# Kernel tuning notes

Measured on AMD Instinct MI355X. Metric: run time of the kernel, lower is better.

The kernel has to match this reference:

```python
import jax, jax.numpy as jnp
import numpy as np
from jax import lax

T, N, E = 12, 10000, 160000
C_IN, C_H, C_OUT = 32, 64, 32
EPS = 1e-5


def _glorot(key, shape):
    fan_in, fan_out = shape[-2] if len(shape) > 1 else shape[0], shape[-1]
    s = (6.0 / (fan_in + fan_out)) ** 0.5
    return jax.random.uniform(key, shape, jnp.float32, -s, s)


def setup_inputs() -> dict:
    key = jax.random.key(0)
    ks = jax.random.split(key, 16)
    inp = {
        "x": jax.random.normal(ks[0], (T, N, C_IN), jnp.float32),
        "edge_index": jax.random.randint(ks[1], (2, E), 0, N, jnp.int32),
        "edge_weight": jax.random.uniform(ks[2], (E,), jnp.float32),
        # layer 1 (input layer): in=C_IN -> C_H
        "conv_w1": _glorot(ks[3], (C_H, C_IN, 3)) * 0.1,
        "conv_b1": jnp.zeros((C_H,), jnp.float32),
        "gamma1": jnp.ones((C_H,), jnp.float32),
        "beta1": jnp.zeros((C_H,), jnp.float32),
        "gcn_w1": _glorot(ks[4], (C_H, C_H)),
        "gcn_b1": jnp.zeros((C_H,), jnp.float32),
        # layer 2 (hidden layer): C_H -> C_H
        "conv_w2": _glorot(ks[5], (C_H, C_H, 3)) * 0.1,
        "conv_b2": jnp.zeros((C_H,), jnp.float32),
        "gamma2": jnp.ones((C_H,), jnp.float32),
        "beta2": jnp.zeros((C_H,), jnp.float32),
        "gcn_w2": _glorot(ks[6], (C_H, C_H)),
        "gcn_b2": jnp.zeros((C_H,), jnp.float32),
        # output linear: C_H -> C_OUT
        "out_w": _glorot(ks[7], (C_H, C_OUT)),
        "out_b": jnp.zeros((C_OUT,), jnp.float32),
    }
    return inp


def _stgcn_layer(x, edge_index, edge_weight, cw, cb, gamma, beta, gw, gb):
    # x: [T, N, C_in]  ->  torch.stack(x).permute(1,2,0) = [N, C_in, T]
    xs = jnp.transpose(x, (1, 2, 0))
    h = lax.conv_general_dilated(xs, cw, (1,), [(1, 1)],
                                 dimension_numbers=("NCH", "OIH", "NCH"))
    h = h + cb[None, :, None]
    # InstanceNorm1d(affine) over the temporal dim
    mu = h.mean(-1, keepdims=True)
    var = ((h - mu) ** 2).mean(-1, keepdims=True)
    h = (h - mu) * lax.rsqrt(var + EPS) * gamma[None, :, None] + beta[None, :, None]
    h = jax.nn.relu(h)
    h = jnp.transpose(h, (2, 0, 1))  # [T, N, C_out]
    # GCNConv per timestep (vectorized over T)
    src, dst = edge_index[0], edge_index[1]
    n = h.shape[1]
    deg = jnp.zeros((n,), h.dtype).at[dst].add(edge_weight) + 1.0  # self-loop weight 1
    dis = lax.rsqrt(deg)
    norm = dis[src] * edge_weight * dis[dst]  # [E]
    xw = jnp.einsum("tnc,cd->tnd", h, gw)  # [T, N, C_out]
    msg = xw[:, src, :] * norm[None, :, None]  # [T, E, C_out]
    agg = jax.vmap(lambda m: jax.ops.segment_sum(m, dst, num_segments=n))(msg)
    agg = agg + (dis * dis)[None, :, None] * xw + gb  # self loop + bias
    return agg


def reference(x, edge_index, edge_weight,
              conv_w1, conv_b1, gamma1, beta1, gcn_w1, gcn_b1,
              conv_w2, conv_b2, gamma2, beta2, gcn_w2, gcn_b2,
              out_w, out_b):
    h = _stgcn_layer(x, edge_index, edge_weight,
                     conv_w1, conv_b1, gamma1, beta1, gcn_w1, gcn_b1)
    h = _stgcn_layer(h, edge_index, edge_weight,
                     conv_w2, conv_b2, gamma2, beta2, gcn_w2, gcn_b2)
    out = jnp.einsum("tnc,co->tno", h, out_w) + out_b  # per-t linear
    return out.mean(axis=0)  # [N, C_OUT]
```

## Files before the change

kernel.cpp:

```cpp
#include <hip/hip_runtime.h>
#include <hip/hip_bf16.h>
#include <stdint.h>

#define MAXDEG 64

typedef short s16x8 __attribute__((ext_vector_type(8)));
typedef short s16x4 __attribute__((ext_vector_type(4)));
typedef float f32x4 __attribute__((ext_vector_type(4)));

static __device__ __forceinline__ float us2f(unsigned short u) {
    union { float f; unsigned int i; } cv; cv.i = ((unsigned int)u) << 16; return cv.f;
}
static __device__ __forceinline__ unsigned short f2us(float f) {
    __hip_bfloat16 h = __float2bfloat16(f);
    return *(unsigned short*)&h;
}

__global__ void k_build_ell(const int* __restrict__ ei, const float* __restrict__ ew,
                            float* __restrict__ deg, unsigned* __restrict__ cnt,
                            int2* __restrict__ ell, int E)
{
    int e = blockIdx.x * 256 + threadIdx.x;
    if (e >= E) return;
    int s = ei[e], d = ei[E + e];
    float w = ew[e];
    atomicAdd(&deg[d], w);
    unsigned slot = atomicAdd(&cnt[d], 1u);
    if (slot < MAXDEG) ell[(size_t)d * MAXDEG + slot] = make_int2(s, __float_as_int(w));
}

__global__ void k_norm(int2* __restrict__ ell, const unsigned* __restrict__ cnt,
                       const float* __restrict__ deg, int N)
{
    int idx = blockIdx.x * 256 + threadIdx.x;
    if (idx >= N * MAXDEG) return;
    int n = idx >> 6;
    int s = idx & (MAXDEG - 1);
    unsigned dg = cnt[n]; if (dg > MAXDEG) dg = MAXDEG;
    int sxo = 0; float nrm = 0.f;
    if ((unsigned)s < dg) {
        int2 p = ell[idx];
        unsigned sx = (unsigned)p.x;
        if (sx < (unsigned)N) {
            nrm = rsqrtf(deg[sx] + 1.0f) * __int_as_float(p.y) * rsqrtf(deg[n] + 1.0f);
            sxo = p.x;
        }
    }
    ell[idx] = make_int2(sxo, __float_as_int(nrm));
}

static __device__ __forceinline__ void edge_acc(float* __restrict__ a, float nrm,
                                                const unsigned short* __restrict__ qp)
{
    ushort4 w0 = *(const ushort4*)qp;
    ushort4 w1 = *(const ushort4*)(qp + 256);
    ushort4 w2 = *(const ushort4*)(qp + 512);
    a[0] = fmaf(nrm, us2f(w0.x), a[0]);  a[1] = fmaf(nrm, us2f(w0.y), a[1]);
    a[2] = fmaf(nrm, us2f(w0.z), a[2]);  a[3] = fmaf(nrm, us2f(w0.w), a[3]);
    a[4] = fmaf(nrm, us2f(w1.x), a[4]);  a[5] = fmaf(nrm, us2f(w1.y), a[5]);
    a[6] = fmaf(nrm, us2f(w1.z), a[6]);  a[7] = fmaf(nrm, us2f(w1.w), a[7]);
    a[8] = fmaf(nrm, us2f(w2.x), a[8]);  a[9] = fmaf(nrm, us2f(w2.y), a[9]);
    a[10] = fmaf(nrm, us2f(w2.z), a[10]); a[11] = fmaf(nrm, us2f(w2.w), a[11]);
}

template<int CIN>
__global__ __launch_bounds__(512, 4) void k_layer_a(
    const float* __restrict__ x_in,
    const float* __restrict__ cw,
    const float* __restrict__ gm, const float* __restrict__ bt,
    const float* __restrict__ gw,
    unsigned short* __restrict__ xw_out, int N)
{
    constexpr int KT   = CIN / 32;
    constexpr int WSTR = (CIN == 64) ? 72 : 40;
    __shared__ __align__(16) short WT[3 * 64 * WSTR];
    __shared__ __align__(16) short gwT[64 * 72];
    __shared__ __align__(16) short xh[8][14 * 72];

    const int tid = threadIdx.x;
    const int nn = tid >> 6;
    const int c = tid & 63;
    const int m = c & 15;
    const int q = c >> 4;
    const int mrow = (m < 12) ? m : 11;
    int n = blockIdx.x * 8 + nn;
    if (n >= N) n = N - 1;

    for (int g = tid; g < 3 * 64 * CIN; g += 512) {
        int kk = g / (64 * CIN);
        int r = g - kk * 64 * CIN;
        int cc = r / CIN, ci = r - cc * CIN;
        WT[kk * (64 * WSTR) + cc * WSTR + ci] = (short)f2us(cw[(cc * CIN + ci) * 3 + kk]);
    }
    for (int g = tid; g < 4096; g += 512) {
        int cc = g >> 6, d = g & 63;
        gwT[d * 72 + cc] = (short)f2us(gw[g]);
    }
    #pragma unroll
    for (int it = 0; it < (12 * CIN) / 64; ++it) {
        int i = it * 64 + c;
        int t = i / CIN, ci = i - t * CIN;
        xh[nn][(t + 1) * 72 + ci] = (short)f2us(x_in[((size_t)t * N + n) * CIN + ci]);
    }
    if (c < CIN) { xh[nn][c] = 0; xh[nn][13 * 72 + c] = 0; }
    __syncthreads();

    f32x4 acc[4];
    #pragma unroll
    for (int nt = 0; nt < 4; ++nt) acc[nt] = (f32x4){0.f, 0.f, 0.f, 0.f};
    #pragma unroll
    for (int kk = 0; kk < 3; ++kk) {
        #pragma unroll
        for (int kt = 0; kt < KT; ++kt) {
            s16x8 aA = *(const s16x8*)&xh[nn][(mrow + kk) * 72 + kt * 32 + q * 8];
            #pragma unroll
            for (int nt = 0; nt < 4; ++nt) {
                s16x8 bB = *(const s16x8*)&WT[kk * (64 * WSTR) + (nt * 16 + m) * WSTR + kt * 32 + q * 8];
                acc[nt] = __builtin_amdgcn_mfma_f32_16x16x32_bf16(aA, bB, acc[nt], 0, 0, 0);
            }
        }
    }

    #pragma unroll
    for (int nt = 0; nt < 4; ++nt) {
        float s  = acc[nt][0] + acc[nt][1] + acc[nt][2] + acc[nt][3];
        float s2 = acc[nt][0] * acc[nt][0] + acc[nt][1] * acc[nt][1]
                 + acc[nt][2] * acc[nt][2] + acc[nt][3] * acc[nt][3];
        if (q == 3) { s = 0.f; s2 = 0.f; }
        s  += __shfl_xor(s, 16);  s  += __shfl_xor(s, 32);
        s2 += __shfl_xor(s2, 16); s2 += __shfl_xor(s2, 32);
        const float mu  = s * (1.f / 12.f);
        const float var = s2 * (1.f / 12.f) - mu * mu;
        const float scn = rsqrtf(var + 1e-5f) * gm[nt * 16 + m];
        const float sbn = bt[nt * 16 + m];
        if (q < 3) {
            #pragma unroll
            for (int reg = 0; reg < 4; ++reg) {
                float h = fmaf(acc[nt][reg] - mu, scn, sbn);
                h = h > 0.f ? h : 0.f;
                xh[nn][(q * 4 + reg) * 72 + nt * 16 + m] = (short)f2us(h);
            }
        }
    }

    s16x8 a2[2];
    #pragma unroll
    for (int kt2 = 0; kt2 < 2; ++kt2)
        a2[kt2] = *(const s16x8*)&xh[nn][mrow * 72 + kt2 * 32 + q * 8];
    f32x4 acc2[4];
    #pragma unroll
    for (int nt = 0; nt < 4; ++nt) acc2[nt] = (f32x4){0.f, 0.f, 0.f, 0.f};
    #pragma unroll
    for (int nt = 0; nt < 4; ++nt) {
        #pragma unroll
        for (int kt2 = 0; kt2 < 2; ++kt2) {
            s16x8 b2 = *(const s16x8*)&gwT[(nt * 16 + m) * 72 + kt2 * 32 + q * 8];
            acc2[nt] = __builtin_amdgcn_mfma_f32_16x16x32_bf16(a2[kt2], b2, acc2[nt], 0, 0, 0);
        }
    }

    unsigned short* dst = xw_out + (size_t)n * 768;
    if (q < 3) {
        #pragma unroll
        for (int nt = 0; nt < 4; ++nt)
            #pragma unroll
            for (int reg = 0; reg < 4; ++reg)
                dst[(q * 4 + reg) * 64 + nt * 16 + m] = f2us(acc2[nt][reg]);
    }
}

__global__ __launch_bounds__(512, 4) void k_gather_a(
    const unsigned short* __restrict__ xw_in,
    const int2* __restrict__ ell, const unsigned* __restrict__ cnt,
    const float* __restrict__ deg, const float* __restrict__ gb,
    const float* __restrict__ cw,
    const float* __restrict__ gm, const float* __restrict__ bt,
    const float* __restrict__ gw,
    unsigned short* __restrict__ rowmean, int N)
{
    constexpr int WSTR = 72;
    __shared__ __align__(16) short WT[3 * 64 * WSTR];
    __shared__ __align__(16) short gwT[64 * 72];
    __shared__ __align__(16) short xh[8][14 * 72];

    const int tid = threadIdx.x;
    const int nn = tid >> 6;
    const int L = tid & 63;
    const int m = L & 15;
    const int q = L >> 4;
    const int mrow = (m < 12) ? m : 11;

    for (int g = tid; g < 3 * 64 * 64; g += 512) {
        int kk = g >> 12;
        int r = g & 4095;
        int cc = r >> 6, ci = r & 63;
        WT[kk * (64 * WSTR) + cc * WSTR + ci] = (short)f2us(cw[(cc * 64 + ci) * 3 + kk]);
    }
    for (int g = tid; g < 4096; g += 512) {
        int cc = g >> 6, d = g & 63;
        gwT[d * 72 + cc] = (short)f2us(gw[g]);
    }
    xh[nn][13 * 72 + L] = 0;
    __syncthreads();

    int base = blockIdx.x * 16 + nn * 2;
    unsigned nP[2];
    nP[0] = (unsigned)((base     < N) ? base     : N - 1);
    nP[1] = (unsigned)((base + 1 < N) ? base + 1 : N - 1);

    float aP[2][12];
    #pragma unroll
    for (int j = 0; j < 2; ++j) {
        const unsigned n = nP[j];
        const float dn = rsqrtf(deg[n] + 1.0f);
        const float d2 = dn * dn;
        const unsigned short* self = xw_in + (size_t)n * 768 + L * 4;
        ushort4 v0 = *(const ushort4*)self;
        ushort4 v1 = *(const ushort4*)(self + 256);
        ushort4 v2 = *(const ushort4*)(self + 512);
        const int c0 = (L * 4) & 63;
        const float g0 = gb[c0], g1 = gb[c0 + 1], g2 = gb[c0 + 2], g3 = gb[c0 + 3];
        float* a = aP[j];
        a[0] = fmaf(d2, us2f(v0.x), g0); a[1] = fmaf(d2, us2f(v0.y), g1);
        a[2] = fmaf(d2, us2f(v0.z), g2); a[3] = fmaf(d2, us2f(v0.w), g3);
        a[4] = fmaf(d2, us2f(v1.x), g0); a[5] = fmaf(d2, us2f(v1.y), g1);
        a[6] = fmaf(d2, us2f(v1.z), g2); a[7] = fmaf(d2, us2f(v1.w), g3);
        a[8] = fmaf(d2, us2f(v2.x), g0); a[9] = fmaf(d2, us2f(v2.y), g1);
        a[10] = fmaf(d2, us2f(v2.z), g2); a[11] = fmaf(d2, us2f(v2.w), g3);
    }
    {
        unsigned dg0 = cnt[nP[0]]; if (dg0 > MAXDEG) dg0 = MAXDEG;
        unsigned dg1 = cnt[nP[1]]; if (dg1 > MAXDEG) dg1 = MAXDEG;
        unsigned dgm = dg0 > dg1 ? dg0 : dg1;
        const int2* r0 = ell + (size_t)nP[0] * MAXDEG;
        const int2* r1 = ell + (size_t)nP[1] * MAXDEG;
        unsigned e = 0;
        for (; e + 2 <= dgm; e += 2) {
            int2 p00 = r0[e], p01 = r0[e + 1], p10 = r1[e], p11 = r1[e + 1];
            edge_acc(aP[0], __int_as_float(p00.y), xw_in + (size_t)(unsigned)p00.x * 768 + L * 4);
            edge_acc(aP[1], __int_as_float(p10.y), xw_in + (size_t)(unsigned)p10.x * 768 + L * 4);
            edge_acc(aP[0], __int_as_float(p01.y), xw_in + (size_t)(unsigned)p01.x * 768 + L * 4);
            edge_acc(aP[1], __int_as_float(p11.y), xw_in + (size_t)(unsigned)p11.x * 768 + L * 4);
        }
        if (e < dgm) {
            int2 p00 = r0[e], p10 = r1[e];
            edge_acc(aP[0], __int_as_float(p00.y), xw_in + (size_t)(unsigned)p00.x * 768 + L * 4);
            edge_acc(aP[1], __int_as_float(p10.y), xw_in + (size_t)(unsigned)p10.x * 768 + L * 4);
        }
    }

    #pragma unroll
    for (int j = 0; j < 2; ++j) {
        const unsigned n = nP[j];
        const float* a = aP[j];

        xh[nn][L] = 0;
        #pragma unroll
        for (int j3 = 0; j3 < 3; ++j3) {
            s16x4 s4 = { (short)f2us(a[j3 * 4 + 0]), (short)f2us(a[j3 * 4 + 1]),
                         (short)f2us(a[j3 * 4 + 2]), (short)f2us(a[j3 * 4 + 3]) };
            *(s16x4*)&xh[nn][(j3 * 4 + q + 1) * 72 + ((L * 4) & 63)] = s4;
        }

        f32x4 acc[4];
        #pragma unroll
        for (int nt = 0; nt < 4; ++nt) acc[nt] = (f32x4){0.f, 0.f, 0.f, 0.f};
        #pragma unroll
        for (int kk = 0; kk < 3; ++kk) {
            #pragma unroll
            for (int kt = 0; kt < 2; ++kt) {
                s16x8 aA = *(const s16x8*)&xh[nn][(mrow + kk) * 72 + kt * 32 + q * 8];
                #pragma unroll
                for (int nt = 0; nt < 4; ++nt) {
                    s16x8 bB = *(const s16x8*)&WT[kk * (64 * WSTR) + (nt * 16 + m) * WSTR + kt * 32 + q * 8];
                    acc[nt] = __builtin_amdgcn_mfma_f32_16x16x32_bf16(aA, bB, acc[nt], 0, 0, 0);
                }
            }
        }

        #pragma unroll
        for (int nt = 0; nt < 4; ++nt) {
            float s  = acc[nt][0] + acc[nt][1] + acc[nt][2] + acc[nt][3];
            float s2 = acc[nt][0] * acc[nt][0] + acc[nt][1] * acc[nt][1]
                     + acc[nt][2] * acc[nt][2] + acc[nt][3] * acc[nt][3];
            if (q == 3) { s = 0.f; s2 = 0.f; }
            s  += __shfl_xor(s, 16);  s  += __shfl_xor(s, 32);
            s2 += __shfl_xor(s2, 16); s2 += __shfl_xor(s2, 32);
            const float mu  = s * (1.f / 12.f);
            const float var = s2 * (1.f / 12.f) - mu * mu;
            const float scn = rsqrtf(var + 1e-5f) * gm[nt * 16 + m];
            const float sbn = bt[nt * 16 + m];
            if (q < 3) {
                #pragma unroll
                for (int reg = 0; reg < 4; ++reg) {
                    float h = fmaf(acc[nt][reg] - mu, scn, sbn);
                    h = h > 0.f ? h : 0.f;
                    xh[nn][(q * 4 + reg) * 72 + nt * 16 + m] = (short)f2us(h);
                }
            }
        }

        s16x8 a2[2];
        #pragma unroll
        for (int kt2 = 0; kt2 < 2; ++kt2)
            a2[kt2] = *(const s16x8*)&xh[nn][mrow * 72 + kt2 * 32 + q * 8];
        f32x4 acc2[4];
        #pragma unroll
        for (int nt = 0; nt < 4; ++nt) acc2[nt] = (f32x4){0.f, 0.f, 0.f, 0.f};
        #pragma unroll
        for (int nt = 0; nt < 4; ++nt) {
            #pragma unroll
            for (int kt2 = 0; kt2 < 2; ++kt2) {
                s16x8 b2 = *(const s16x8*)&gwT[(nt * 16 + m) * 72 + kt2 * 32 + q * 8];
                acc2[nt] = __builtin_amdgcn_mfma_f32_16x16x32_bf16(a2[kt2], b2, acc2[nt], 0, 0, 0);
            }
        }

        #pragma unroll
        for (int nt = 0; nt < 4; ++nt) {
            float pm = (q < 3) ? (acc2[nt][0] + acc2[nt][1] + acc2[nt][2] + acc2[nt][3]) : 0.f;
            pm += __shfl_xor(pm, 16); pm += __shfl_xor(pm, 32);
            if (q == 0)
                rowmean[(size_t)n * 64 + nt * 16 + m] = f2us(pm * (1.f / 12.f));
        }
    }
}

__global__ __launch_bounds__(256) void k_final(
    const unsigned short* __restrict__ rowmean, const int2* __restrict__ ell,
    const unsigned* __restrict__ cnt, const float* __restrict__ deg,
    const float* __restrict__ gb,
    const float* __restrict__ ow, const float* __restrict__ ob,
    float* __restrict__ dout, int N)
{
    __shared__ __align__(16) float hbuf[4][64];
    const int tid = threadIdx.x;
    const int nn = tid >> 6, L = tid & 63;
    int n = blockIdx.x * 4 + nn;
    if (n >= N) n = N - 1;
    const float dn = rsqrtf(deg[n] + 1.0f);
    const float d2 = dn * dn;

    float a = fmaf(d2, us2f(rowmean[(size_t)n * 64 + L]), gb[L]);

    unsigned dg = cnt[n]; if (dg > MAXDEG) dg = MAXDEG;
    const int2* row = ell + (size_t)n * MAXDEG;
    unsigned e = 0;
    for (; e + 8 <= dg; e += 8) {
        #pragma unroll
        for (int i = 0; i < 8; ++i) {
            int2 p = row[e + i];
            a = fmaf(__int_as_float(p.y), us2f(rowmean[(size_t)(unsigned)p.x * 64 + L]), a);
        }
    }
    for (; e < dg; ++e) {
        int2 p = row[e];
        a = fmaf(__int_as_float(p.y), us2f(rowmean[(size_t)(unsigned)p.x * 64 + L]), a);
    }

    hbuf[nn][L] = a;
    __syncthreads();
    if (L < 32) {
        float oa = ob[L];
        #pragma unroll
        for (int cc = 0; cc < 64; ++cc)
            oa = fmaf(hbuf[nn][cc], ow[cc * 32 + L], oa);
        dout[(size_t)n * 32 + L] = oa;
    }
}

extern "C" void kernel_launch(void* const* d_in, const int* in_sizes, int n_in,
                              void* d_out, int out_size, void* d_ws, size_t ws_size,
                              hipStream_t stream)
{
    const float* x   = (const float*)d_in[0];
    const int*   ei  = (const int*)d_in[1];
    const float* ew  = (const float*)d_in[2];
    const float* cw1 = (const float*)d_in[3];
    const float* gm1 = (const float*)d_in[5];
    const float* bt1 = (const float*)d_in[6];
    const float* gw1 = (const float*)d_in[7];
    const float* gb1 = (const float*)d_in[8];
    const float* cw2 = (const float*)d_in[9];
    const float* gm2 = (const float*)d_in[11];
    const float* bt2 = (const float*)d_in[12];
    const float* gw2 = (const float*)d_in[13];
    const float* gb2 = (const float*)d_in[14];
    const float* ow  = (const float*)d_in[15];
    const float* ob  = (const float*)d_in[16];

    const int N = in_sizes[0] / (12 * 32);
    const int E = in_sizes[2];

    char* p0 = (char*)d_ws;
    char* p = p0;
    float* deg = (float*)p;          p += (size_t)N * 4;
    unsigned* cnt = (unsigned*)p;    p += (size_t)N * 4;
    p = (char*)(((uintptr_t)p + 255) & ~(uintptr_t)255);
    int2* ell = (int2*)p;            p += (size_t)N * MAXDEG * 8;
    p = (char*)(((uintptr_t)p + 255) & ~(uintptr_t)255);
    unsigned short* bufXW1 = (unsigned short*)p; p += (size_t)N * 768 * 2;
    unsigned short* rowmean = (unsigned short*)p; p += (size_t)N * 64 * 2;

    const size_t need = (size_t)(p - p0);
    if (ws_size < need) {
        hipMemsetAsync(d_out, 0, (size_t)out_size * 4, stream);
        return;
    }

    hipMemsetAsync(deg, 0, (size_t)N * 8, stream);

    const int eb   = (E + 255) / 256;
    const int nb8  = (N + 7) / 8;
    const int nb16 = (N + 15) / 16;
    const int nb4  = (N + 3) / 4;
    k_build_ell<<<eb, 256, 0, stream>>>(ei, ew, deg, cnt, ell, E);
    k_norm<<<(N * MAXDEG + 255) / 256, 256, 0, stream>>>(ell, cnt, deg, N);

    k_layer_a<32><<<nb8, 512, 0, stream>>>(x, cw1, gm1, bt1, gw1, bufXW1, N);
    k_gather_a<<<nb16, 512, 0, stream>>>(bufXW1, ell, cnt, deg, gb1,
                                         cw2, gm2, bt2, gw2, rowmean, N);
    k_final<<<nb4, 256, 0, stream>>>(rowmean, ell, cnt, deg, gb2, ow, ob, (float*)d_out, N);
}
```

Measured before the change: 196.7 us.

## Use persistent grid-stride blocks and batched 8-edge gather in layer kernels

Both MFMA layer kernels now launch a fixed grid (1024 and 768 blocks) and loop over node groups grid-stride, so the per-block staging of conv and GCN weights into LDS is paid once per block, not once per small node group. The gather kernel now assigns one node per wavefront instead of two, and walks the padded ELL row in chunks of 8 edges with all loads issued before the FMAs, to raise memory-level parallelism. Padding to a multiple of 8 relies on the zeroed padding entries in the ELL table, which adds some wasted loads of row 0. The fixed grid sizes may leave the GPU underfilled or unevenly loaded.

```diff
diff --git a/kernel.cpp b/kernel.cpp
--- a/kernel.cpp
+++ b/kernel.cpp
@@ -49,20 +49,6 @@
     ell[idx] = make_int2(sxo, __float_as_int(nrm));
 }
 
-static __device__ __forceinline__ void edge_acc(float* __restrict__ a, float nrm,
-                                                const unsigned short* __restrict__ qp)
-{
-    ushort4 w0 = *(const ushort4*)qp;
-    ushort4 w1 = *(const ushort4*)(qp + 256);
-    ushort4 w2 = *(const ushort4*)(qp + 512);
-    a[0] = fmaf(nrm, us2f(w0.x), a[0]);  a[1] = fmaf(nrm, us2f(w0.y), a[1]);
-    a[2] = fmaf(nrm, us2f(w0.z), a[2]);  a[3] = fmaf(nrm, us2f(w0.w), a[3]);
-    a[4] = fmaf(nrm, us2f(w1.x), a[4]);  a[5] = fmaf(nrm, us2f(w1.y), a[5]);
-    a[6] = fmaf(nrm, us2f(w1.z), a[6]);  a[7] = fmaf(nrm, us2f(w1.w), a[7]);
-    a[8] = fmaf(nrm, us2f(w2.x), a[8]);  a[9] = fmaf(nrm, us2f(w2.y), a[9]);
-    a[10] = fmaf(nrm, us2f(w2.z), a[10]); a[11] = fmaf(nrm, us2f(w2.w), a[11]);
-}
-
 template<int CIN>
 __global__ __launch_bounds__(512, 4) void k_layer_a(
     const float* __restrict__ x_in,
@@ -83,8 +69,6 @@
     const int m = c & 15;
     const int q = c >> 4;
     const int mrow = (m < 12) ? m : 11;
-    int n = blockIdx.x * 8 + nn;
-    if (n >= N) n = N - 1;
 
     for (int g = tid; g < 3 * 64 * CIN; g += 512) {
         int kk = g / (64 * CIN);
@@ -96,170 +80,19 @@
         int cc = g >> 6, d = g & 63;
         gwT[d * 72 + cc] = (short)f2us(gw[g]);
     }
-    #pragma unroll
-    for (int it = 0; it < (12 * CIN) / 64; ++it) {
-        int i = it * 64 + c;
-        int t = i / CIN, ci = i - t * CIN;
-        xh[nn][(t + 1) * 72 + ci] = (short)f2us(x_in[((size_t)t * N + n) * CIN + ci]);
-    }
-    if (c < CIN) { xh[nn][c] = 0; xh[nn][13 * 72 + c] = 0; }
+    if (c < CIN) xh[nn][13 * 72 + c] = 0;
     __syncthreads();
 
-    f32x4 acc[4];
-    #pragma unroll
-    for (int nt = 0; nt < 4; ++nt) acc[nt] = (f32x4){0.f, 0.f, 0.f, 0.f};
-    #pragma unroll
-    for (int kk = 0; kk < 3; ++kk) {
-        #pragma unroll
-        for (int kt = 0; kt < KT; ++kt) {
-            s16x8 aA = *(const s16x8*)&xh[nn][(mrow + kk) * 72 + kt * 32 + q * 8];
-            #pragma unroll
-            for (int nt = 0; nt < 4; ++nt) {
-                s16x8 bB = *(const s16x8*)&WT[kk * (64 * WSTR) + (nt * 16 + m) * WSTR + kt * 32 + q * 8];
-                acc[nt] = __builtin_amdgcn_mfma_f32_16x16x32_bf16(aA, bB, acc[nt], 0, 0, 0);
-            }
-        }
-    }
-
-    #pragma unroll
-    for (int nt = 0; nt < 4; ++nt) {
-        float s  = acc[nt][0] + acc[nt][1] + acc[nt][2] + acc[nt][3];
-        float s2 = acc[nt][0] * acc[nt][0] + acc[nt][1] * acc[nt][1]
-                 + acc[nt][2] * acc[nt][2] + acc[nt][3] * acc[nt][3];
-        if (q == 3) { s = 0.f; s2 = 0.f; }
-        s  += __shfl_xor(s, 16);  s  += __shfl_xor(s, 32);
-        s2 += __shfl_xor(s2, 16); s2 += __shfl_xor(s2, 32);
-        const float mu  = s * (1.f / 12.f);
-        const float var = s2 * (1.f / 12.f) - mu * mu;
-        const float scn = rsqrtf(var + 1e-5f) * gm[nt * 16 + m];
-        const float sbn = bt[nt * 16 + m];
-        if (q < 3) {
-            #pragma unroll
-            for (int reg = 0; reg < 4; ++reg) {
-                float h = fmaf(acc[nt][reg] - mu, scn, sbn);
-                h = h > 0.f ? h : 0.f;
-                xh[nn][(q * 4 + reg) * 72 + nt * 16 + m] = (short)f2us(h);
-            }
-        }
-    }
-
-    s16x8 a2[2];
-    #pragma unroll
-    for (int kt2 = 0; kt2 < 2; ++kt2)
-        a2[kt2] = *(const s16x8*)&xh[nn][mrow * 72 + kt2 * 32 + q * 8];
-    f32x4 acc2[4];
-    #pragma unroll
-    for (int nt = 0; nt < 4; ++nt) acc2[nt] = (f32x4){0.f, 0.f, 0.f, 0.f};
-    #pragma unroll
-    for (int nt = 0; nt < 4; ++nt) {
-        #pragma unroll
-        for (int kt2 = 0; kt2 < 2; ++kt2) {
-            s16x8 b2 = *(const s16x8*)&gwT[(nt * 16 + m) * 72 + kt2 * 32 + q * 8];
-            acc2[nt] = __builtin_amdgcn_mfma_f32_16x16x32_bf16(a2[kt2], b2, acc2[nt], 0, 0, 0);
-        }
-    }
-
-    unsigned short* dst = xw_out + (size_t)n * 768;
-    if (q < 3) {
-        #pragma unroll
-        for (int nt = 0; nt < 4; ++nt)
-            #pragma unroll
-            for (int reg = 0; reg < 4; ++reg)
-                dst[(q * 4 + reg) * 64 + nt * 16 + m] = f2us(acc2[nt][reg]);
-    }
-}
-
-__global__ __launch_bounds__(512, 4) void k_gather_a(
-    const unsigned short* __restrict__ xw_in,
-    const int2* __restrict__ ell, const unsigned* __restrict__ cnt,
-    const float* __restrict__ deg, const float* __restrict__ gb,
-    const float* __restrict__ cw,
-    const float* __restrict__ gm, const float* __restrict__ bt,
-    const float* __restrict__ gw,
-    unsigned short* __restrict__ rowmean, int N)
-{
-    constexpr int WSTR = 72;
-    __shared__ __align__(16) short WT[3 * 64 * WSTR];
-    __shared__ __align__(16) short gwT[64 * 72];
-    __shared__ __align__(16) short xh[8][14 * 72];
-
-    const int tid = threadIdx.x;
-    const int nn = tid >> 6;
-    const int L = tid & 63;
-    const int m = L & 15;
-    const int q = L >> 4;
-    const int mrow = (m < 12) ? m : 11;
-
-    for (int g = tid; g < 3 * 64 * 64; g += 512) {
-        int kk = g >> 12;
-        int r = g & 4095;
-        int cc = r >> 6, ci = r & 63;
-        WT[kk * (64 * WSTR) + cc * WSTR + ci] = (short)f2us(cw[(cc * 64 + ci) * 3 + kk]);
-    }
-    for (int g = tid; g < 4096; g += 512) {
-        int cc = g >> 6, d = g & 63;
-        gwT[d * 72 + cc] = (short)f2us(gw[g]);
-    }
-    xh[nn][13 * 72 + L] = 0;
-    __syncthreads();
-
-    int base = blockIdx.x * 16 + nn * 2;
-    unsigned nP[2];
-    nP[0] = (unsigned)((base     < N) ? base     : N - 1);
-    nP[1] = (unsigned)((base + 1 < N) ? base + 1 : N - 1);
-
-    float aP[2][12];
-    #pragma unroll
-    for (int j = 0; j < 2; ++j) {
-        const unsigned n = nP[j];
-        const float dn = rsqrtf(deg[n] + 1.0f);
-        const float d2 = dn * dn;
-        const unsigned short* self = xw_in + (size_t)n * 768 + L * 4;
-        ushort4 v0 = *(const ushort4*)self;
-        ushort4 v1 = *(const ushort4*)(self + 256);
-        ushort4 v2 = *(const ushort4*)(self + 512);
-        const int c0 = (L * 4) & 63;
-        const float g0 = gb[c0], g1 = gb[c0 + 1], g2 = gb[c0 + 2], g3 = gb[c0 + 3];
-        float* a = aP[j];
-        a[0] = fmaf(d2, us2f(v0.x), g0); a[1] = fmaf(d2, us2f(v0.y), g1);
-        a[2] = fmaf(d2, us2f(v0.z), g2); a[3] = fmaf(d2, us2f(v0.w), g3);
-        a[4] = fmaf(d2, us2f(v1.x), g0); a[5] = fmaf(d2, us2f(v1.y), g1);
-        a[6] = fmaf(d2, us2f(v1.z), g2); a[7] = fmaf(d2, us2f(v1.w), g3);
-        a[8] = fmaf(d2, us2f(v2.x), g0); a[9] = fmaf(d2, us2f(v2.y), g1);
-        a[10] = fmaf(d2, us2f(v2.z), g2); a[11] = fmaf(d2, us2f(v2.w), g3);
-    }
-    {
-        unsigned dg0 = cnt[nP[0]]; if (dg0 > MAXDEG) dg0 = MAXDEG;
-        unsigned dg1 = cnt[nP[1]]; if (dg1 > MAXDEG) dg1 = MAXDEG;
-        unsigned dgm = dg0 > dg1 ? dg0 : dg1;
-        const int2* r0 = ell + (size_t)nP[0] * MAXDEG;
-        const int2* r1 = ell + (size_t)nP[1] * MAXDEG;
-        unsigned e = 0;
-        for (; e + 2 <= dgm; e += 2) {
-            int2 p00 = r0[e], p01 = r0[e + 1], p10 = r1[e], p11 = r1[e + 1];
-            edge_acc(aP[0], __int_as_float(p00.y), xw_in + (size_t)(unsigned)p00.x * 768 + L * 4);
-            edge_acc(aP[1], __int_as_float(p10.y), xw_in + (size_t)(unsigned)p10.x * 768 + L * 4);
-            edge_acc(aP[0], __int_as_float(p01.y), xw_in + (size_t)(unsigned)p01.x * 768 + L * 4);
-            edge_acc(aP[1], __int_as_float(p11.y), xw_in + (size_t)(unsigned)p11.x * 768 + L * 4);
-        }
-        if (e < dgm) {
-            int2 p00 = r0[e], p10 = r1[e];
-            edge_acc(aP[0], __int_as_float(p00.y), xw_in + (size_t)(unsigned)p00.x * 768 + L * 4);
-            edge_acc(aP[1], __int_as_float(p10.y), xw_in + (size_t)(unsigned)p10.x * 768 + L * 4);
-        }
-    }
-
-    #pragma unroll
-    for (int j = 0; j < 2; ++j) {
-        const unsigned n = nP[j];
-        const float* a = aP[j];
-
-        xh[nn][L] = 0;
-        #pragma unroll
-        for (int j3 = 0; j3 < 3; ++j3) {
-            s16x4 s4 = { (short)f2us(a[j3 * 4 + 0]), (short)f2us(a[j3 * 4 + 1]),
-                         (short)f2us(a[j3 * 4 + 2]), (short)f2us(a[j3 * 4 + 3]) };
-            *(s16x4*)&xh[nn][(j3 * 4 + q + 1) * 72 + ((L * 4) & 63)] = s4;
+    for (int base = blockIdx.x * 8; base < N; base += gridDim.x * 8) {
+        int n = base + nn;
+        if (n >= N) n = N - 1;
+
+        if (c < CIN) xh[nn][c] = 0;
+        #pragma unroll
+        for (int it = 0; it < (12 * CIN) / 64; ++it) {
+            int i = it * 64 + c;
+            int t = i / CIN, ci = i - t * CIN;
+            xh[nn][(t + 1) * 72 + ci] = (short)f2us(x_in[((size_t)t * N + n) * CIN + ci]);
         }
 
         f32x4 acc[4];
@@ -268,7 +101,7 @@
         #pragma unroll
         for (int kk = 0; kk < 3; ++kk) {
             #pragma unroll
-            for (int kt = 0; kt < 2; ++kt) {
+            for (int kt = 0; kt < KT; ++kt) {
                 s16x8 aA = *(const s16x8*)&xh[nn][(mrow + kk) * 72 + kt * 32 + q * 8];
                 #pragma unroll
                 for (int nt = 0; nt < 4; ++nt) {
@@ -316,6 +149,161 @@
             }
         }
 
+        unsigned short* dst = xw_out + (size_t)n * 768;
+        if (q < 3) {
+            #pragma unroll
+            for (int nt = 0; nt < 4; ++nt)
+                #pragma unroll
+                for (int reg = 0; reg < 4; ++reg)
+                    dst[(q * 4 + reg) * 64 + nt * 16 + m] = f2us(acc2[nt][reg]);
+        }
+    }
+}
+
+__global__ __launch_bounds__(512, 4) void k_gather_a(
+    const unsigned short* __restrict__ xw_in,
+    const int2* __restrict__ ell, const unsigned* __restrict__ cnt,
+    const float* __restrict__ deg, const float* __restrict__ gb,
+    const float* __restrict__ cw,
+    const float* __restrict__ gm, const float* __restrict__ bt,
+    const float* __restrict__ gw,
+    unsigned short* __restrict__ rowmean, int N)
+{
+    constexpr int WSTR = 72;
+    __shared__ __align__(16) short WT[3 * 64 * WSTR];
+    __shared__ __align__(16) short gwT[64 * 72];
+    __shared__ __align__(16) short xh[8][14 * 72];
+
+    const int tid = threadIdx.x;
+    const int nn = tid >> 6;
+    const int L = tid & 63;
+    const int m = L & 15;
+    const int q = L >> 4;
+    const int mrow = (m < 12) ? m : 11;
+
+    for (int g = tid; g < 3 * 64 * 64; g += 512) {
+        int kk = g >> 12;
+        int r = g & 4095;
+        int cc = r >> 6, ci = r & 63;
+        WT[kk * (64 * WSTR) + cc * WSTR + ci] = (short)f2us(cw[(cc * 64 + ci) * 3 + kk]);
+    }
+    for (int g = tid; g < 4096; g += 512) {
+        int cc = g >> 6, d = g & 63;
+        gwT[d * 72 + cc] = (short)f2us(gw[g]);
+    }
+    xh[nn][13 * 72 + L] = 0;
+    __syncthreads();
+
+    for (int base = blockIdx.x * 8; base < N; base += gridDim.x * 8) {
+        int ni = base + nn;
+        if (ni >= N) ni = N - 1;
+        const unsigned n = (unsigned)ni;
+
+        const float dn = rsqrtf(deg[n] + 1.0f);
+        const float d2 = dn * dn;
+        float a[12];
+        {
+            const unsigned short* self = xw_in + (size_t)n * 768 + L * 4;
+            ushort4 v0 = *(const ushort4*)self;
+            ushort4 v1 = *(const ushort4*)(self + 256);
+            ushort4 v2 = *(const ushort4*)(self + 512);
+            const int c0 = (L * 4) & 63;
+            const float g0 = gb[c0], g1 = gb[c0 + 1], g2 = gb[c0 + 2], g3 = gb[c0 + 3];
+            a[0] = fmaf(d2, us2f(v0.x), g0); a[1] = fmaf(d2, us2f(v0.y), g1);
+            a[2] = fmaf(d2, us2f(v0.z), g2); a[3] = fmaf(d2, us2f(v0.w), g3);
+            a[4] = fmaf(d2, us2f(v1.x), g0); a[5] = fmaf(d2, us2f(v1.y), g1);
+            a[6] = fmaf(d2, us2f(v1.z), g2); a[7] = fmaf(d2, us2f(v1.w), g3);
+            a[8] = fmaf(d2, us2f(v2.x), g0); a[9] = fmaf(d2, us2f(v2.y), g1);
+            a[10] = fmaf(d2, us2f(v2.z), g2); a[11] = fmaf(d2, us2f(v2.w), g3);
+        }
+        unsigned dg = cnt[n]; if (dg > MAXDEG) dg = MAXDEG;
+        const unsigned dgp = (dg + 7u) & ~7u;
+        const int2* row = ell + (size_t)n * MAXDEG;
+        for (unsigned e = 0; e < dgp; e += 8) {
+            ushort4 v[8][3]; float nf[8];
+            #pragma unroll
+            for (int i = 0; i < 8; ++i) {
+                int2 p = row[e + i];
+                nf[i] = __int_as_float(p.y);
+                const unsigned short* qp = xw_in + (size_t)(unsigned)p.x * 768 + L * 4;
+                v[i][0] = *(const ushort4*)qp;
+                v[i][1] = *(const ushort4*)(qp + 256);
+                v[i][2] = *(const ushort4*)(qp + 512);
+            }
+            #pragma unroll
+            for (int i = 0; i < 8; ++i) {
+                const float nrm = nf[i];
+                a[0] = fmaf(nrm, us2f(v[i][0].x), a[0]);  a[1] = fmaf(nrm, us2f(v[i][0].y), a[1]);
+                a[2] = fmaf(nrm, us2f(v[i][0].z), a[2]);  a[3] = fmaf(nrm, us2f(v[i][0].w), a[3]);
+                a[4] = fmaf(nrm, us2f(v[i][1].x), a[4]);  a[5] = fmaf(nrm, us2f(v[i][1].y), a[5]);
+                a[6] = fmaf(nrm, us2f(v[i][1].z), a[6]);  a[7] = fmaf(nrm, us2f(v[i][1].w), a[7]);
+                a[8] = fmaf(nrm, us2f(v[i][2].x), a[8]);  a[9] = fmaf(nrm, us2f(v[i][2].y), a[9]);
+                a[10] = fmaf(nrm, us2f(v[i][2].z), a[10]); a[11] = fmaf(nrm, us2f(v[i][2].w), a[11]);
+            }
+        }
+
+        xh[nn][L] = 0;
+        #pragma unroll
+        for (int j3 = 0; j3 < 3; ++j3) {
+            s16x4 s4 = { (short)f2us(a[j3 * 4 + 0]), (short)f2us(a[j3 * 4 + 1]),
+                         (short)f2us(a[j3 * 4 + 2]), (short)f2us(a[j3 * 4 + 3]) };
+            *(s16x4*)&xh[nn][(j3 * 4 + q + 1) * 72 + ((L * 4) & 63)] = s4;
+        }
+
+        f32x4 acc[4];
+        #pragma unroll
+        for (int nt = 0; nt < 4; ++nt) acc[nt] = (f32x4){0.f, 0.f, 0.f, 0.f};
+        #pragma unroll
+        for (int kk = 0; kk < 3; ++kk) {
+            #pragma unroll
+            for (int kt = 0; kt < 2; ++kt) {
+                s16x8 aA = *(const s16x8*)&xh[nn][(mrow + kk) * 72 + kt * 32 + q * 8];
+                #pragma unroll
+                for (int nt = 0; nt < 4; ++nt) {
+                    s16x8 bB = *(const s16x8*)&WT[kk * (64 * WSTR) + (nt * 16 + m) * WSTR + kt * 32 + q * 8];
+                    acc[nt] = __builtin_amdgcn_mfma_f32_16x16x32_bf16(aA, bB, acc[nt], 0, 0, 0);
+                }
+            }
+        }
+
+        #pragma unroll
+        for (int nt = 0; nt < 4; ++nt) {
+            float s  = acc[nt][0] + acc[nt][1] + acc[nt][2] + acc[nt][3];
+            float s2 = acc[nt][0] * acc[nt][0] + acc[nt][1] * acc[nt][1]
+                     + acc[nt][2] * acc[nt][2] + acc[nt][3] * acc[nt][3];
+            if (q == 3) { s = 0.f; s2 = 0.f; }
+            s  += __shfl_xor(s, 16);  s  += __shfl_xor(s, 32);
+            s2 += __shfl_xor(s2, 16); s2 += __shfl_xor(s2, 32);
+            const float mu  = s * (1.f / 12.f);
+            const float var = s2 * (1.f / 12.f) - mu * mu;
+            const float scn = rsqrtf(var + 1e-5f) * gm[nt * 16 + m];
+            const float sbn = bt[nt * 16 + m];
+            if (q < 3) {
+                #pragma unroll
+                for (int reg = 0; reg < 4; ++reg) {
+                    float h = fmaf(acc[nt][reg] - mu, scn, sbn);
+                    h = h > 0.f ? h : 0.f;
+                    xh[nn][(q * 4 + reg) * 72 + nt * 16 + m] = (short)f2us(h);
+                }
+            }
+        }
+
+        s16x8 a2[2];
+        #pragma unroll
+        for (int kt2 = 0; kt2 < 2; ++kt2)
+            a2[kt2] = *(const s16x8*)&xh[nn][mrow * 72 + kt2 * 32 + q * 8];
+        f32x4 acc2[4];
+        #pragma unroll
+        for (int nt = 0; nt < 4; ++nt) acc2[nt] = (f32x4){0.f, 0.f, 0.f, 0.f};
+        #pragma unroll
+        for (int nt = 0; nt < 4; ++nt) {
+            #pragma unroll
+            for (int kt2 = 0; kt2 < 2; ++kt2) {
+                s16x8 b2 = *(const s16x8*)&gwT[(nt * 16 + m) * 72 + kt2 * 32 + q * 8];
+                acc2[nt] = __builtin_amdgcn_mfma_f32_16x16x32_bf16(a2[kt2], b2, acc2[nt], 0, 0, 0);
+            }
+        }
+
         #pragma unroll
         for (int nt = 0; nt < 4; ++nt) {
             float pm = (q < 3) ? (acc2[nt][0] + acc2[nt][1] + acc2[nt][2] + acc2[nt][3]) : 0.f;
@@ -410,15 +398,13 @@
 
     hipMemsetAsync(deg, 0, (size_t)N * 8, stream);
 
-    const int eb   = (E + 255) / 256;
-    const int nb8  = (N + 7) / 8;
-    const int nb16 = (N + 15) / 16;
-    const int nb4  = (N + 3) / 4;
+    const int eb  = (E + 255) / 256;
+    const int nb4 = (N + 3) / 4;
     k_build_ell<<<eb, 256, 0, stream>>>(ei, ew, deg, cnt, ell, E);
     k_norm<<<(N * MAXDEG + 255) / 256, 256, 0, stream>>>(ell, cnt, deg, N);
 
-    k_layer_a<32><<<nb8, 512, 0, stream>>>(x, cw1, gm1, bt1, gw1, bufXW1, N);
-    k_gather_a<<<nb16, 512, 0, stream>>>(bufXW1, ell, cnt, deg, gb1,
-                                         cw2, gm2, bt2, gw2, rowmean, N);
+    k_layer_a<32><<<1024, 512, 0, stream>>>(x, cw1, gm1, bt1, gw1, bufXW1, N);
+    k_gather_a<<<768, 512, 0, stream>>>(bufXW1, ell, cnt, deg, gb1,
+                                        cw2, gm2, bt2, gw2, rowmean, N);
     k_final<<<nb4, 256, 0, stream>>>(rowmean, ell, cnt, deg, gb2, ow, ob, (float*)d_out, N);
 }
```

Measured after the change: 274.1 us. +39.4%, slower.
